# Optimization experiments

Hardware: AMD Instinct MI355X
Metric: run time of the kernel (lower is better)

Reference implementation:

```python
import jax, jax.numpy as jnp
import numpy as np

DIM = 1024
HEADS = 16
DIM_HEAD = 64
CHUNK = 64
INNER = HEADS * DIM_HEAD  # 1024


def setup_inputs() -> dict:
    key = jax.random.key(0)
    k1, k2, k3 = jax.random.split(key, 3)
    x = jax.random.normal(k1, (4, 4096, DIM), dtype=jnp.float32)
    # nn.Linear weights stored as (out, in); apply as x @ W.T
    w_qkv = jax.random.normal(k2, (INNER * 3, DIM), dtype=jnp.float32) * (DIM ** -0.5)
    w_out = jax.random.normal(k3, (DIM, INNER), dtype=jnp.float32) * (INNER ** -0.5)
    b_out = jnp.zeros((DIM,), dtype=jnp.float32)
    return {"x": x, "w_qkv": w_qkv, "w_out": w_out, "b_out": b_out}


def reference(x, w_qkv, w_out, b_out):
    b, n, _ = x.shape
    scale = DIM_HEAD ** -0.5
    qkv = jnp.einsum('bnd,ed->bne', x, w_qkv)  # (b, n, 3*inner)
    q, k, v = jnp.split(qkv, 3, axis=-1)
    nblk = n // CHUNK

    def to_blocks(t):
        # (b, n, h*d) -> (b, h, nblk, c, d)
        t = t.reshape(b, n, HEADS, DIM_HEAD).transpose(0, 2, 1, 3)
        return t.reshape(b, HEADS, nblk, CHUNK, DIM_HEAD)

    qb, kb, vb = to_blocks(q), to_blocks(k), to_blocks(v)
    scores = jnp.einsum('bhgqd,bhgkd->bhgqk', qb, kb) * scale  # block-local
    attn = jax.nn.softmax(scores, axis=-1)
    ob = jnp.einsum('bhgqk,bhgkd->bhgqd', attn, vb)
    out = ob.reshape(b, HEADS, n, DIM_HEAD).transpose(0, 2, 1, 3).reshape(b, n, INNER)
    return jnp.einsum('bne,de->bnd', out, w_out) + b_out
```

## Files before the change

### kernel.cpp

```cpp
#include <hip/hip_runtime.h>
#include <stdint.h>

typedef __attribute__((ext_vector_type(8))) short bf16x8;
typedef __attribute__((ext_vector_type(4))) float f32x4;

__device__ __forceinline__ unsigned short bf16_of(float f) {
  union { float f; uint32_t u; } x; x.f = f;
  uint32_t r = x.u + 0x7fffu + ((x.u >> 16) & 1u);
  return (unsigned short)(r >> 16);
}

#define GLD16(gp, lp) __builtin_amdgcn_global_load_lds( \
    (const __attribute__((address_space(1))) uint32_t*)(gp), \
    (__attribute__((address_space(3))) uint32_t*)(lp), 16, 0, 0)

#define BAR() do { asm volatile("" ::: "memory"); __builtin_amdgcn_s_barrier(); asm volatile("" ::: "memory"); } while (0)

__global__ void cvt_f32_bf16(const float* __restrict__ src,
                             unsigned short* __restrict__ dst, int n4) {
  int i = blockIdx.x * blockDim.x + threadIdx.x;
  int stride = gridDim.x * blockDim.x;
  for (int j = i; j < n4; j += stride) {
    float4 f = ((const float4*)src)[j];
    union { unsigned short s[4]; uint2 v; } u;
    u.s[0] = bf16_of(f.x); u.s[1] = bf16_of(f.y);
    u.s[2] = bf16_of(f.z); u.s[3] = bf16_of(f.w);
    ((uint2*)dst)[j] = u.v;
  }
}

template<int BIAS, int OUTF32, int GW, int NSEG>
__global__ __launch_bounds__(512, 2)
void gemm256p(const unsigned short* __restrict__ A,
              const unsigned short* __restrict__ B,
              void* __restrict__ C, const float* __restrict__ bias,
              int N, int K)
{
  __shared__ __align__(1024) unsigned short sm[65536];
  char* const smb = (char*)sm;
  const int tid = threadIdx.x, w = tid >> 6, lane = tid & 63;
  const int wm = w >> 2, wn = w & 3;
  const int fr = lane & 15, kg = lane >> 4;
  const int swz = (fr & 7) << 4;
  const int srow = lane >> 3, sslot = lane & 7;
  const int cXcd = blockIdx.x & 7, iIdx = blockIdx.x >> 3;
  const int NT_tot = NSEG * 16;

  auto tileMN = [&](int s, int& mt, int& nt) {
    const int T = cXcd * (32 * NSEG) + s * 32 + iIdx;
    const int g = T / (64 * GW), rr = T % (64 * GW);
    mt = rr / GW; nt = g * GW + rr % GW;
  };

  auto STAGE = [&](int u, int opnd, int half) {
    int mt, nt; tileMN(u >> 4, mt, nt);
    const unsigned short* G_ = opnd ? B : A;
    const int grow0 = (opnd ? nt : mt) << 8;
    char* region = smb + opnd * 65536 + (u & 1) * 32768 + half * 16384;
    const int k0 = (u & 15) << 6;
    #pragma unroll
    for (int i2 = 0; i2 < 2; ++i2) {
      const int c = i2 * 8 + w;
      const int row = half * 128 + c * 8 + srow;
      const int slot = sslot ^ srow;
      GLD16(G_ + (size_t)(grow0 + row) * K + k0 + slot * 8, region + c * 1024);
    }
  };
  auto LDA = [&](char* Ab, int j, int ks) -> bf16x8 {
    const int r = 32 * j + 16 * wm + fr;
    return *(const bf16x8*)(Ab + r * 128 + ((ks * 64 + kg * 16) ^ swz));
  };
  auto LDB = [&](char* Bb, int l, int ks) -> bf16x8 {
    const int r = 64 * l + 16 * wn + fr;
    return *(const bf16x8*)(Bb + r * 128 + ((ks * 64 + kg * 16) ^ swz));
  };

  f32x4 acc[8][4] = {};

  STAGE(0, 0, 0); STAGE(0, 1, 0); STAGE(0, 0, 1); STAGE(0, 1, 1);
  STAGE(1, 0, 0); STAGE(1, 1, 1); STAGE(1, 0, 1);
  asm volatile("s_waitcnt vmcnt(6)" ::: "memory");
  BAR();

  for (int s = 0; s < NSEG; ++s) {
    for (int tt = 0; tt < 16; ++tt) {
      const int G = s * 16 + tt;
      char* Ab = smb + (G & 1) * 32768;
      char* Bb = smb + 65536 + (G & 1) * 32768;
      bf16x8 a[4][2], b[2][2], b0[2][2];

      #pragma unroll
      for (int j = 0; j < 4; ++j) { a[j][0] = LDA(Ab, j, 0); a[j][1] = LDA(Ab, j, 1); }
      #pragma unroll
      for (int l = 0; l < 2; ++l) { b0[l][0] = LDB(Bb, l, 0); b0[l][1] = LDB(Bb, l, 1); }
      if (G + 1 < NT_tot) STAGE(G + 1, 1, 0);
      BAR();
      __builtin_amdgcn_s_setprio(1);
      #pragma unroll
      for (int j = 0; j < 4; ++j)
        #pragma unroll
        for (int l = 0; l < 2; ++l) {
          acc[j][l] = __builtin_amdgcn_mfma_f32_16x16x32_bf16(a[j][0], b0[l][0], acc[j][l], 0, 0, 0);
          acc[j][l] = __builtin_amdgcn_mfma_f32_16x16x32_bf16(a[j][1], b0[l][1], acc[j][l], 0, 0, 0);
        }
      __builtin_amdgcn_s_setprio(0);
      BAR();

      #pragma unroll
      for (int l = 0; l < 2; ++l) { b[l][0] = LDB(Bb, l + 2, 0); b[l][1] = LDB(Bb, l + 2, 1); }
      if (G + 2 < NT_tot) STAGE(G + 2, 0, 0);
      BAR();
      __builtin_amdgcn_s_setprio(1);
      #pragma unroll
      for (int j = 0; j < 4; ++j)
        #pragma unroll
        for (int l = 0; l < 2; ++l) {
          acc[j][l + 2] = __builtin_amdgcn_mfma_f32_16x16x32_bf16(a[j][0], b[l][0], acc[j][l + 2], 0, 0, 0);
          acc[j][l + 2] = __builtin_amdgcn_mfma_f32_16x16x32_bf16(a[j][1], b[l][1], acc[j][l + 2], 0, 0, 0);
        }
      __builtin_amdgcn_s_setprio(0);
      BAR();

      #pragma unroll
      for (int j = 0; j < 4; ++j) { a[j][0] = LDA(Ab, j + 4, 0); a[j][1] = LDA(Ab, j + 4, 1); }
      if (G + 2 < NT_tot) STAGE(G + 2, 1, 1);
      BAR();
      __builtin_amdgcn_s_setprio(1);
      #pragma unroll
      for (int j = 0; j < 4; ++j)
        #pragma unroll
        for (int l = 0; l < 2; ++l) {
          acc[j + 4][l + 2] = __builtin_amdgcn_mfma_f32_16x16x32_bf16(a[j][0], b[l][0], acc[j + 4][l + 2], 0, 0, 0);
          acc[j + 4][l + 2] = __builtin_amdgcn_mfma_f32_16x16x32_bf16(a[j][1], b[l][1], acc[j + 4][l + 2], 0, 0, 0);
        }
      __builtin_amdgcn_s_setprio(0);
      BAR();

      if (G + 2 < NT_tot) STAGE(G + 2, 0, 1);
      BAR();
      __builtin_amdgcn_s_setprio(1);
      #pragma unroll
      for (int j = 0; j < 4; ++j)
        #pragma unroll
        for (int l = 0; l < 2; ++l) {
          acc[j + 4][l] = __builtin_amdgcn_mfma_f32_16x16x32_bf16(a[j][0], b0[l][0], acc[j + 4][l], 0, 0, 0);
          acc[j + 4][l] = __builtin_amdgcn_mfma_f32_16x16x32_bf16(a[j][1], b0[l][1], acc[j + 4][l], 0, 0, 0);
        }
      __builtin_amdgcn_s_setprio(0);
      if (G == NT_tot - 2)      { asm volatile("s_waitcnt vmcnt(0)" ::: "memory"); }
      else if (G < NT_tot - 2)  { asm volatile("s_waitcnt vmcnt(6)" ::: "memory"); }
      BAR();
    }

    int mt, nt; tileMN(s, mt, nt);
    const int bm0 = mt << 8, bn0 = nt << 8;
    #pragma unroll
    for (int l = 0; l < 4; ++l) {
      const int col = bn0 + 64 * l + 16 * wn + fr;
      float bb = 0.0f;
      if (BIAS && OUTF32) bb = bias[col];
      #pragma unroll
      for (int j = 0; j < 8; ++j) {
        const int row0 = bm0 + 32 * j + 16 * wm + kg * 4;
        #pragma unroll
        for (int rr = 0; rr < 4; ++rr) {
          if (OUTF32)
            ((float*)C)[(size_t)(row0 + rr) * N + col] = acc[j][l][rr] + bb;
          else
            ((unsigned short*)C)[(size_t)(row0 + rr) * N + col] = bf16_of(acc[j][l][rr]);
        }
      }
    }
    #pragma unroll
    for (int j = 0; j < 8; ++j)
      #pragma unroll
      for (int l = 0; l < 4; ++l)
        acc[j][l] = f32x4{0.f, 0.f, 0.f, 0.f};
  }
}

__global__ __launch_bounds__(256, 2)
void attn_block(const unsigned short* __restrict__ qkv,
                unsigned short* __restrict__ o)
{
  __shared__ __align__(1024) unsigned short Qs[64 * 64];
  __shared__ __align__(1024) unsigned short Ks[64 * 64];
  __shared__ __align__(1024) unsigned short Vt[64 * 64];
  __shared__ __align__(1024) unsigned short Ps[64 * 64];
  const int tid = threadIdx.x, w = tid >> 6, lane = tid & 63;
  const int g = blockIdx.x, h = blockIdx.y, b = blockIdx.z;
  const size_t mbase = (size_t)b * 4096 + (size_t)g * 64;
  const unsigned short* qg = qkv + mbase * 3072 + h * 64;
  const unsigned short* kgl = qkv + mbase * 3072 + 1024 + h * 64;
  const unsigned short* vg = qkv + mbase * 3072 + 2048 + h * 64;

  #pragma unroll
  for (int i = 0; i < 2; ++i) {
    const int chunk = i * 4 + w;
    const int row = chunk * 8 + (lane >> 3);
    const int c8 = (lane & 7) ^ (row & 7);
    GLD16(qg + (size_t)row * 3072 + c8 * 8, (char*)Qs + chunk * 1024);
    GLD16(kgl + (size_t)row * 3072 + c8 * 8, (char*)Ks + chunk * 1024);
  }
  #pragma unroll
  for (int i = 0; i < 2; ++i) {
    const int c = i * 256 + tid;
    const int n = c >> 3, d0 = (c & 7) * 8;
    bf16x8 v = *(const bf16x8*)(vg + (size_t)n * 3072 + d0);
    #pragma unroll
    for (int j = 0; j < 8; ++j) {
      const int d = d0 + j;
      const int bo = d * 128 + n * 2;
      *(unsigned short*)((char*)Vt + (bo ^ ((d & 7) << 4))) = (unsigned short)v[j];
    }
  }
  __syncthreads();

  const int fr = lane & 15, kg = lane >> 4;
  f32x4 s[4] = {};
  #pragma unroll
  for (int kt = 0; kt < 2; ++kt) {
    const int kb = kt * 64 + kg * 16;
    const int rq = w * 16 + fr;
    bf16x8 aq = *(const bf16x8*)((const char*)Qs + rq * 128 + (kb ^ ((rq & 7) << 4)));
    #pragma unroll
    for (int nf = 0; nf < 4; ++nf) {
      const int rk = nf * 16 + fr;
      bf16x8 bk = *(const bf16x8*)((const char*)Ks + rk * 128 + (kb ^ ((rk & 7) << 4)));
      s[nf] = __builtin_amdgcn_mfma_f32_16x16x32_bf16(aq, bk, s[nf], 0, 0, 0);
    }
  }

  const float scale = 0.125f;
  float inv[4];
  #pragma unroll
  for (int r = 0; r < 4; ++r) {
    float m0 = fmaxf(fmaxf(s[0][r], s[1][r]), fmaxf(s[2][r], s[3][r]));
    #pragma unroll
    for (int d = 1; d < 16; d <<= 1) m0 = fmaxf(m0, __shfl_xor(m0, d));
    float sum = 0.0f;
    #pragma unroll
    for (int nf = 0; nf < 4; ++nf) {
      float p = __expf((s[nf][r] - m0) * scale);
      s[nf][r] = p;
      sum += p;
    }
    #pragma unroll
    for (int d = 1; d < 16; d <<= 1) sum += __shfl_xor(sum, d);
    inv[r] = 1.0f / sum;
  }

  #pragma unroll
  for (int r = 0; r < 4; ++r) {
    const int m = w * 16 + kg * 4 + r;
    #pragma unroll
    for (int nf = 0; nf < 4; ++nf) {
      const int bo = m * 128 + (nf * 16 + fr) * 2;
      *(unsigned short*)((char*)Ps + (bo ^ ((m & 7) << 4))) = bf16_of(s[nf][r] * inv[r]);
    }
  }
  __syncthreads();

  f32x4 oa[4] = {};
  #pragma unroll
  for (int kt = 0; kt < 2; ++kt) {
    const int kb = kt * 64 + kg * 16;
    const int rp = w * 16 + fr;
    bf16x8 ap = *(const bf16x8*)((const char*)Ps + rp * 128 + (kb ^ ((rp & 7) << 4)));
    #pragma unroll
    for (int df = 0; df < 4; ++df) {
      const int rv = df * 16 + fr;
      bf16x8 bv = *(const bf16x8*)((const char*)Vt + rv * 128 + (kb ^ ((rv & 7) << 4)));
      oa[df] = __builtin_amdgcn_mfma_f32_16x16x32_bf16(ap, bv, oa[df], 0, 0, 0);
    }
  }
  #pragma unroll
  for (int df = 0; df < 4; ++df) {
    #pragma unroll
    for (int r = 0; r < 4; ++r) {
      const size_t row = mbase + w * 16 + kg * 4 + r;
      const int col = h * 64 + df * 16 + fr;
      o[row * 1024 + col] = bf16_of(oa[df][r]);
    }
  }
}

extern "C" void kernel_launch(void* const* d_in, const int* in_sizes, int n_in,
                              void* d_out, int out_size, void* d_ws, size_t ws_size,
                              hipStream_t stream) {
  const float* x     = (const float*)d_in[0];
  const float* w_qkv = (const float*)d_in[1];
  const float* w_out = (const float*)d_in[2];
  const float* b_out = (const float*)d_in[3];
  char* ws = (char*)d_ws;
  const size_t SZ_X  = (size_t)16384 * 1024 * 2;
  const size_t SZ_WQ = (size_t)3072 * 1024 * 2;
  const size_t SZ_WO = (size_t)1024 * 1024 * 2;
  unsigned short* xb  = (unsigned short*)ws;
  unsigned short* wqb = (unsigned short*)(ws + SZ_X);
  unsigned short* wob = (unsigned short*)(ws + SZ_X + SZ_WQ);
  unsigned short* qkv = (unsigned short*)(ws + SZ_X + SZ_WQ + SZ_WO);
  unsigned short* ob  = xb;

  cvt_f32_bf16<<<2048, 256, 0, stream>>>(x, xb, 16384 * 1024 / 4);
  cvt_f32_bf16<<<512, 256, 0, stream>>>(w_qkv, wqb, 3072 * 1024 / 4);
  cvt_f32_bf16<<<256, 256, 0, stream>>>(w_out, wob, 1024 * 1024 / 4);
  gemm256p<0,0,6,3><<<dim3(256), 512, 0, stream>>>(xb, wqb, qkv, nullptr, 3072, 1024);
  attn_block<<<dim3(64, 16, 4), 256, 0, stream>>>(qkv, ob);
  gemm256p<1,1,4,1><<<dim3(256), 512, 0, stream>>>(ob, wob, d_out, b_out, 1024, 1024);
}
```

Measured before the change: 197.6 us.

## Restructure GEMM main loop to prefetch whole next tile with two barriers

```diff
diff --git a/kernel.cpp b/kernel.cpp
--- a/kernel.cpp
+++ b/kernel.cpp
@@ -31,7 +31,7 @@
 
 template<int BIAS, int OUTF32, int GW, int NSEG>
 __global__ __launch_bounds__(512, 2)
-void gemm256p(const unsigned short* __restrict__ A,
+void gemm256f(const unsigned short* __restrict__ A,
               const unsigned short* __restrict__ B,
               void* __restrict__ C, const float* __restrict__ bias,
               int N, int K)
@@ -77,24 +77,31 @@
 
   f32x4 acc[8][4] = {};
 
-  STAGE(0, 0, 0); STAGE(0, 1, 0); STAGE(0, 0, 1); STAGE(0, 1, 1);
-  STAGE(1, 0, 0); STAGE(1, 1, 1); STAGE(1, 0, 1);
-  asm volatile("s_waitcnt vmcnt(6)" ::: "memory");
-  BAR();
+  STAGE(0, 1, 0); STAGE(0, 0, 0); STAGE(0, 1, 1); STAGE(0, 0, 1);
 
   for (int s = 0; s < NSEG; ++s) {
     for (int tt = 0; tt < 16; ++tt) {
-      const int G = s * 16 + tt;
-      char* Ab = smb + (G & 1) * 32768;
-      char* Bb = smb + 65536 + (G & 1) * 32768;
-      bf16x8 a[4][2], b[2][2], b0[2][2];
-
+      const int T = s * 16 + tt;
+      char* Ab = smb + (T & 1) * 32768;
+      char* Bb = smb + 65536 + (T & 1) * 32768;
+      bf16x8 a[4][2], b0[2][2], b1[2][2];
+
+      asm volatile("s_waitcnt vmcnt(2)" ::: "memory");
+      BAR();
+
+      if (T + 1 < NT_tot) {
+        STAGE(T + 1, 1, 0);
+        STAGE(T + 1, 0, 0);
+        STAGE(T + 1, 1, 1);
+        STAGE(T + 1, 0, 1);
+      }
+
+      #pragma unroll
+      for (int l = 0; l < 2; ++l) { b0[l][0] = LDB(Bb, l, 0); b0[l][1] = LDB(Bb, l, 1); }
       #pragma unroll
       for (int j = 0; j < 4; ++j) { a[j][0] = LDA(Ab, j, 0); a[j][1] = LDA(Ab, j, 1); }
       #pragma unroll
-      for (int l = 0; l < 2; ++l) { b0[l][0] = LDB(Bb, l, 0); b0[l][1] = LDB(Bb, l, 1); }
-      if (G + 1 < NT_tot) STAGE(G + 1, 1, 0);
-      BAR();
+      for (int l = 0; l < 2; ++l) { b1[l][0] = LDB(Bb, l + 2, 0); b1[l][1] = LDB(Bb, l + 2, 1); }
       __builtin_amdgcn_s_setprio(1);
       #pragma unroll
       for (int j = 0; j < 4; ++j)
@@ -103,42 +110,28 @@
           acc[j][l] = __builtin_amdgcn_mfma_f32_16x16x32_bf16(a[j][0], b0[l][0], acc[j][l], 0, 0, 0);
           acc[j][l] = __builtin_amdgcn_mfma_f32_16x16x32_bf16(a[j][1], b0[l][1], acc[j][l], 0, 0, 0);
         }
+      #pragma unroll
+      for (int j = 0; j < 4; ++j)
+        #pragma unroll
+        for (int l = 0; l < 2; ++l) {
+          acc[j][l + 2] = __builtin_amdgcn_mfma_f32_16x16x32_bf16(a[j][0], b1[l][0], acc[j][l + 2], 0, 0, 0);
+          acc[j][l + 2] = __builtin_amdgcn_mfma_f32_16x16x32_bf16(a[j][1], b1[l][1], acc[j][l + 2], 0, 0, 0);
+        }
       __builtin_amdgcn_s_setprio(0);
+
+      asm volatile("s_waitcnt vmcnt(8)" ::: "memory");
       BAR();
 
       #pragma unroll
-      for (int l = 0; l < 2; ++l) { b[l][0] = LDB(Bb, l + 2, 0); b[l][1] = LDB(Bb, l + 2, 1); }
-      if (G + 2 < NT_tot) STAGE(G + 2, 0, 0);
-      BAR();
+      for (int j = 0; j < 4; ++j) { a[j][0] = LDA(Ab, j + 4, 0); a[j][1] = LDA(Ab, j + 4, 1); }
       __builtin_amdgcn_s_setprio(1);
       #pragma unroll
       for (int j = 0; j < 4; ++j)
         #pragma unroll
         for (int l = 0; l < 2; ++l) {
-          acc[j][l + 2] = __builtin_amdgcn_mfma_f32_16x16x32_bf16(a[j][0], b[l][0], acc[j][l + 2], 0, 0, 0);
-          acc[j][l + 2] = __builtin_amdgcn_mfma_f32_16x16x32_bf16(a[j][1], b[l][1], acc[j][l + 2], 0, 0, 0);
-        }
-      __builtin_amdgcn_s_setprio(0);
-      BAR();
-
-      #pragma unroll
-      for (int j = 0; j < 4; ++j) { a[j][0] = LDA(Ab, j + 4, 0); a[j][1] = LDA(Ab, j + 4, 1); }
-      if (G + 2 < NT_tot) STAGE(G + 2, 1, 1);
-      BAR();
-      __builtin_amdgcn_s_setprio(1);
-      #pragma unroll
-      for (int j = 0; j < 4; ++j)
-        #pragma unroll
-        for (int l = 0; l < 2; ++l) {
-          acc[j + 4][l + 2] = __builtin_amdgcn_mfma_f32_16x16x32_bf16(a[j][0], b[l][0], acc[j + 4][l + 2], 0, 0, 0);
-          acc[j + 4][l + 2] = __builtin_amdgcn_mfma_f32_16x16x32_bf16(a[j][1], b[l][1], acc[j + 4][l + 2], 0, 0, 0);
-        }
-      __builtin_amdgcn_s_setprio(0);
-      BAR();
-
-      if (G + 2 < NT_tot) STAGE(G + 2, 0, 1);
-      BAR();
-      __builtin_amdgcn_s_setprio(1);
+          acc[j + 4][l + 2] = __builtin_amdgcn_mfma_f32_16x16x32_bf16(a[j][0], b1[l][0], acc[j + 4][l + 2], 0, 0, 0);
+          acc[j + 4][l + 2] = __builtin_amdgcn_mfma_f32_16x16x32_bf16(a[j][1], b1[l][1], acc[j + 4][l + 2], 0, 0, 0);
+        }
       #pragma unroll
       for (int j = 0; j < 4; ++j)
         #pragma unroll
@@ -147,9 +140,6 @@
           acc[j + 4][l] = __builtin_amdgcn_mfma_f32_16x16x32_bf16(a[j][1], b0[l][1], acc[j + 4][l], 0, 0, 0);
         }
       __builtin_amdgcn_s_setprio(0);
-      if (G == NT_tot - 2)      { asm volatile("s_waitcnt vmcnt(0)" ::: "memory"); }
-      else if (G < NT_tot - 2)  { asm volatile("s_waitcnt vmcnt(6)" ::: "memory"); }
-      BAR();
     }
 
     int mt, nt; tileMN(s, mt, nt);
@@ -305,7 +295,7 @@
   cvt_f32_bf16<<<2048, 256, 0, stream>>>(x, xb, 16384 * 1024 / 4);
   cvt_f32_bf16<<<512, 256, 0, stream>>>(w_qkv, wqb, 3072 * 1024 / 4);
   cvt_f32_bf16<<<256, 256, 0, stream>>>(w_out, wob, 1024 * 1024 / 4);
-  gemm256p<0,0,6,3><<<dim3(256), 512, 0, stream>>>(xb, wqb, qkv, nullptr, 3072, 1024);
+  gemm256f<0,0,6,3><<<dim3(256), 512, 0, stream>>>(xb, wqb, qkv, nullptr, 3072, 1024);
   attn_block<<<dim3(64, 16, 4), 256, 0, stream>>>(qkv, ob);
-  gemm256p<1,1,4,1><<<dim3(256), 512, 0, stream>>>(ob, wob, d_out, b_out, 1024, 1024);
-}
+  gemm256f<1,1,4,1><<<dim3(256), 512, 0, stream>>>(ob, wob, d_out, b_out, 1024, 1024);
+}
```

Result: faster. 185.4 us (-6.2%).
